# Kernel tuning notes

Measured on AMD Instinct MI355X. Metric: run time of the kernel, lower is better.

Reference implementation:

```python
import jax, jax.numpy as jnp
import numpy as np

B, S, E, H, F = 4, 2048, 1024, 16, 4096
D = E // H
EPS = 1e-5


def setup_inputs() -> dict:
    key = jax.random.key(0)
    ks = jax.random.split(key, 12)
    sc_e = 1.0 / np.sqrt(E)
    sc_f = 1.0 / np.sqrt(F)
    inp = {
        'x': jax.random.normal(ks[0], (B, S, E), jnp.float32),
        'mask': jnp.tril(jnp.ones((S, S), jnp.int32))[None, None],  # causal [1,1,S,S]
        'ln1_g': jnp.ones((E,), jnp.float32),
        'ln1_b': jnp.zeros((E,), jnp.float32),
        'Wq': jax.random.normal(ks[1], (E, E), jnp.float32) * sc_e,
        'bq': jnp.zeros((E,), jnp.float32),
        'Wk': jax.random.normal(ks[2], (E, E), jnp.float32) * sc_e,
        'bk': jnp.zeros((E,), jnp.float32),
        'Wv': jax.random.normal(ks[3], (E, E), jnp.float32) * sc_e,
        'bv': jnp.zeros((E,), jnp.float32),
        'Wo': jax.random.normal(ks[4], (E, E), jnp.float32) * sc_e,
        'bo': jnp.zeros((E,), jnp.float32),
        'ln2_g': jnp.ones((E,), jnp.float32),
        'ln2_b': jnp.zeros((E,), jnp.float32),
        'W1': jax.random.normal(ks[5], (F, E), jnp.float32) * sc_e,
        'b1': jnp.zeros((F,), jnp.float32),
        'W2': jax.random.normal(ks[6], (E, F), jnp.float32) * sc_f,
        'b2': jnp.zeros((E,), jnp.float32),
    }
    return inp


def _ln(x, g, b):
    m = jnp.mean(x, axis=-1, keepdims=True)
    v = jnp.mean(jnp.square(x - m), axis=-1, keepdims=True)
    return (x - m) * jax.lax.rsqrt(v + EPS) * g + b


def _attn(h, mask, Wq, bq, Wk, bk, Wv, bv, Wo, bo):
    b, s, _ = h.shape
    q = (h @ Wq.T + bq).reshape(b, s, H, D)
    k = (h @ Wk.T + bk).reshape(b, s, H, D)
    v = (h @ Wv.T + bv).reshape(b, s, H, D)
    scores = jnp.einsum('bqhd,bkhd->bhqk', q, k) / np.sqrt(D)
    scores = jnp.where(mask == 0, -jnp.inf, scores)
    w = jax.nn.softmax(scores, axis=-1)
    ctx = jnp.einsum('bhqk,bkhd->bqhd', w, v).reshape(b, s, E)
    return ctx @ Wo.T + bo


def reference(x, mask, ln1_g, ln1_b, Wq, bq, Wk, bk, Wv, bv, Wo, bo,
              ln2_g, ln2_b, W1, b1, W2, b2):
    x = x + _attn(_ln(x, ln1_g, ln1_b), mask, Wq, bq, Wk, bk, Wv, bv, Wo, bo)
    h = _ln(x, ln2_g, ln2_b)
    ffn = jax.nn.gelu(h @ W1.T + b1, approximate=False) @ W2.T + b2
    return x + ffn
```

## Files before the change

kernel.cpp:

```cpp
#include <hip/hip_runtime.h>
#include <cstdint>
#include <cstddef>

#define E_DIM 1024
#define F_DIM 4096
#define S_LEN 2048
#define NB    4
#define NH    16
#define HD    64
#define MROWS 8192

typedef __bf16 bf16x8 __attribute__((ext_vector_type(8)));
typedef float  f32x4  __attribute__((ext_vector_type(4)));

struct alignas(16) f4 { float x, y, z, w; };
__device__ __forceinline__ f4 ld4(const float* p){ return *(const f4*)p; }

__device__ __forceinline__ unsigned short f2bf(float f){
  union { float f; unsigned int u; } c; c.f = f;
  unsigned int u = c.u;
  return (unsigned short)((u + 0x7FFFu + ((u >> 16) & 1u)) >> 16);
}

__device__ __forceinline__ float gelu_fast(float v){
  const float x  = v * 0.70710678118654752f;
  const float ax = fabsf(x);
  const float t  = __builtin_amdgcn_rcpf(1.0f + 0.3275911f * ax);
  const float p  = t*(0.254829592f + t*(-0.284496736f + t*(1.421413741f +
                   t*(-1.453152027f + t*1.061405429f))));
  float er = 1.0f - p * __expf(-x * x);
  er = (x < 0.0f) ? -er : er;
  return 0.5f * v * (1.0f + er);
}

__device__ __forceinline__ void xcd_swz(int gx, int gy, int& bn, int& bm){
  int fid = blockIdx.y * gx + blockIdx.x;
  const int nwg = gx * gy;
  fid = (fid & 7) * (nwg >> 3) + (fid >> 3);
  bn = fid % gx; bm = fid / gx;
}

__global__ void cvt_kernel(const float* __restrict__ in, unsigned short* __restrict__ out,
                           int n, float scale){
  int i = (blockIdx.x * 256 + threadIdx.x) * 4;
  if (i >= n) return;
  f4 f = ld4(in + i);
  ushort4 o;
  o.x = f2bf(f.x * scale); o.y = f2bf(f.y * scale);
  o.z = f2bf(f.z * scale); o.w = f2bf(f.w * scale);
  *(ushort4*)(out + i) = o;
}

__global__ void bias_cat(const float* __restrict__ bq, const float* __restrict__ bk,
                         const float* __restrict__ bv, float* __restrict__ out, float qsc){
  int i = blockIdx.x * 256 + threadIdx.x;
  if (i >= 3 * E_DIM) return;
  float v = (i < E_DIM) ? bq[i] * qsc : (i < 2 * E_DIM ? bk[i - E_DIM] : bv[i - 2 * E_DIM]);
  out[i] = v;
}

__global__ __launch_bounds__(256) void ln_kernel(const float* __restrict__ in,
                                                 const float* __restrict__ g,
                                                 const float* __restrict__ b,
                                                 unsigned short* __restrict__ out){
  const int row = blockIdx.x;
  const int t = threadIdx.x;
  const float* xr = in + (size_t)row * E_DIM;
  f4 xv = ld4(xr + t * 4);
  float s  = xv.x + xv.y + xv.z + xv.w;
  float ss = xv.x*xv.x + xv.y*xv.y + xv.z*xv.z + xv.w*xv.w;
  #pragma unroll
  for (int o = 1; o < 64; o <<= 1){ s += __shfl_xor(s, o); ss += __shfl_xor(ss, o); }
  __shared__ float sa[4], sb[4];
  if ((t & 63) == 0){ sa[t >> 6] = s; sb[t >> 6] = ss; }
  __syncthreads();
  s  = sa[0] + sa[1] + sa[2] + sa[3];
  ss = sb[0] + sb[1] + sb[2] + sb[3];
  const float mean = s * (1.0f / E_DIM);
  const float var  = ss * (1.0f / E_DIM) - mean * mean;
  const float rstd = rsqrtf(var + 1e-5f);
  f4 gv = ld4(g + t * 4);
  f4 bv = ld4(b + t * 4);
  ushort4 o;
  o.x = f2bf((xv.x - mean) * rstd * gv.x + bv.x);
  o.y = f2bf((xv.y - mean) * rstd * gv.y + bv.y);
  o.z = f2bf((xv.z - mean) * rstd * gv.z + bv.z);
  o.w = f2bf((xv.w - mean) * rstd * gv.w + bv.w);
  *(ushort4*)(out + (size_t)row * E_DIM + t * 4) = o;
}

__device__ __forceinline__ void async_cp16(const unsigned short* g, unsigned short* l){
  __builtin_amdgcn_global_load_lds((const __attribute__((address_space(1))) unsigned int*)g,
                                   (__attribute__((address_space(3)))       unsigned int*)l,
                                   16, 0, 0);
}

template<int EPI>
__global__ __launch_bounds__(256) void gemm_bt(const unsigned short* __restrict__ A,
                                               const unsigned short* __restrict__ W,
                                               const float* __restrict__ bias,
                                               const float* __restrict__ res,
                                               void* __restrict__ outp,
                                               int M, int N, int K){
  __shared__ unsigned short As[128 * 64];
  __shared__ unsigned short Bs[128 * 64];
  int bn, bm; xcd_swz(gridDim.x, gridDim.y, bn, bm);
  const int tid = threadIdx.x;
  const int wv = tid >> 6, lane = tid & 63;
  const int lr = lane & 15, qd = lane >> 4;
  const int wm = (wv >> 1) * 64, wn = (wv & 1) * 64;

  f32x4 acc[4][4];
  #pragma unroll
  for (int mt = 0; mt < 4; ++mt)
    #pragma unroll
    for (int nt = 0; nt < 4; ++nt)
      acc[mt][nt] = f32x4{0.f, 0.f, 0.f, 0.f};

  int soff[4];
  int srow[4];
  #pragma unroll
  for (int it = 0; it < 4; ++it){
    const int cc = tid + it * 256;
    srow[it] = cc >> 3;
    soff[it] = (((cc & 7) ^ (srow[it] & 7))) * 8;
  }
  const unsigned short* Abase = A + (size_t)(bm * 128) * K;
  const unsigned short* Wbase = W + (size_t)(bn * 128) * K;

  for (int k0 = 0; k0 < K; k0 += 64){
    __syncthreads();
    #pragma unroll
    for (int it = 0; it < 4; ++it){
      async_cp16(Abase + (size_t)srow[it] * K + k0 + soff[it], &As[(tid + it * 256) * 8]);
      async_cp16(Wbase + (size_t)srow[it] * K + k0 + soff[it], &Bs[(tid + it * 256) * 8]);
    }
    __builtin_amdgcn_s_waitcnt(0);
    __syncthreads();

    #pragma unroll
    for (int kk = 0; kk < 2; ++kk){
      bf16x8 af[4], bf[4];
      #pragma unroll
      for (int mt = 0; mt < 4; ++mt){
        const int fr = wm + mt * 16 + lr;
        af[mt] = *(const bf16x8*)&As[fr * 64 + (((kk * 4 + qd) ^ (fr & 7))) * 8];
      }
      #pragma unroll
      for (int nt = 0; nt < 4; ++nt){
        const int fr = wn + nt * 16 + lr;
        bf[nt] = *(const bf16x8*)&Bs[fr * 64 + (((kk * 4 + qd) ^ (fr & 7))) * 8];
      }
      #pragma unroll
      for (int mt = 0; mt < 4; ++mt)
        #pragma unroll
        for (int nt = 0; nt < 4; ++nt)
          acc[mt][nt] = __builtin_amdgcn_mfma_f32_16x16x32_bf16(af[mt], bf[nt], acc[mt][nt], 0, 0, 0);
    }
  }

  #pragma unroll
  for (int mt = 0; mt < 4; ++mt){
    #pragma unroll
    for (int r = 0; r < 4; ++r){
      const int gm = bm * 128 + wm + mt * 16 + qd * 4 + r;
      const size_t rowoff = (size_t)gm * N;
      #pragma unroll
      for (int nt = 0; nt < 4; ++nt){
        const int gn = bn * 128 + wn + nt * 16 + lr;
        float v = acc[mt][nt][r] + bias[gn];
        if constexpr (EPI == 1) v = gelu_fast(v);
        if constexpr (EPI == 2) ((float*)outp)[rowoff + gn] = v + res[rowoff + gn];
        else                    ((unsigned short*)outp)[rowoff + gn] = f2bf(v);
      }
    }
  }
}

#define VMW4() asm volatile("s_waitcnt vmcnt(4)" ::: "memory")
#define VMW0() asm volatile("s_waitcnt vmcnt(0)" ::: "memory")
#define BAR()  __builtin_amdgcn_s_barrier()

template<int EPI>
__global__ __launch_bounds__(512, 2) void gemm256(const unsigned short* __restrict__ A,
                                                  const unsigned short* __restrict__ W,
                                                  const float* __restrict__ bias,
                                                  unsigned short* __restrict__ outp,
                                                  int M, int N, int K){
  __shared__ unsigned short lds[2][2][256 * 64];
  const int bn = blockIdx.x, bm = blockIdx.y;
  const int tid = threadIdx.x;
  const int lane = tid & 63;
  const int wv = tid >> 6;
  const int lr = lane & 15, qd = lane >> 4;
  const int wm = wv >> 2, wn = wv & 3;
  const int NT = K >> 6;

  f32x4 acc[2][2][4][2];
  #pragma unroll
  for (int a = 0; a < 2; ++a)
    #pragma unroll
    for (int b = 0; b < 2; ++b)
      #pragma unroll
      for (int c = 0; c < 4; ++c)
        #pragma unroll
        for (int d = 0; d < 2; ++d)
          acc[a][b][c][d] = f32x4{0.f, 0.f, 0.f, 0.f};

  const int srow = tid >> 3;
  const int scol = ((tid & 7) ^ (srow & 7)) * 8;
  const unsigned short* Ab = A + (size_t)(bm * 256 + srow) * K + scol;
  const unsigned short* Wb = W + (size_t)(bn * 256 + srow) * K + scol;

#define STAGE_A(bufi, h, kt) do{ \
    async_cp16(Ab + (size_t)((h)*128     ) * K + (size_t)(kt) * 64, &lds[bufi][0][((h)*128     ) * 64 + tid * 8]); \
    async_cp16(Ab + (size_t)((h)*128 + 64) * K + (size_t)(kt) * 64, &lds[bufi][0][((h)*128 + 64) * 64 + tid * 8]); \
  }while(0)
#define STAGE_B(bufi, h, kt) do{ \
    async_cp16(Wb + (size_t)((h)*128     ) * K + (size_t)(kt) * 64, &lds[bufi][1][((h)*128     ) * 64 + tid * 8]); \
    async_cp16(Wb + (size_t)((h)*128 + 64) * K + (size_t)(kt) * 64, &lds[bufi][1][((h)*128 + 64) * 64 + tid * 8]); \
  }while(0)

  const int sw0 = ((qd    ) ^ (lr & 7)) * 8;
  const int sw1 = ((qd + 4) ^ (lr & 7)) * 8;
  const int arow = wm * 64 + lr;
  const int brow = wn * 32 + lr;

  bf16x8 af[4][2], b0[2][2], b1[2][2];

#define LDA(bufi, mh) do{ \
    _Pragma("unroll") \
    for (int mt = 0; mt < 4; ++mt){ \
      const int r_ = (mh)*128 + arow + mt * 16; \
      af[mt][0] = *(const bf16x8*)&lds[bufi][0][r_ * 64 + sw0]; \
      af[mt][1] = *(const bf16x8*)&lds[bufi][0][r_ * 64 + sw1]; \
    } }while(0)
#define LDB(bufi, nh, dst) do{ \
    _Pragma("unroll") \
    for (int nt = 0; nt < 2; ++nt){ \
      const int r_ = (nh)*128 + brow + nt * 16; \
      dst[nt][0] = *(const bf16x8*)&lds[bufi][1][r_ * 64 + sw0]; \
      dst[nt][1] = *(const bf16x8*)&lds[bufi][1][r_ * 64 + sw1]; \
    } }while(0)
#define MMA(mh, nh, bfr) do{ \
    __builtin_amdgcn_s_setprio(1); \
    _Pragma("unroll") \
    for (int kk = 0; kk < 2; ++kk) \
      _Pragma("unroll") \
      for (int mt = 0; mt < 4; ++mt) \
        _Pragma("unroll") \
        for (int nt = 0; nt < 2; ++nt) \
          acc[mh][nh][mt][nt] = __builtin_amdgcn_mfma_f32_16x16x32_bf16(af[mt][kk], bfr[nt][kk], acc[mh][nh][mt][nt], 0, 0, 0); \
    __builtin_amdgcn_s_setprio(0); \
  }while(0)

  STAGE_A(0, 0, 0); STAGE_B(0, 1, 0); STAGE_A(0, 1, 0); STAGE_B(0, 0, 0);
  STAGE_A(1, 0, 1); STAGE_B(1, 1, 1);
  VMW4(); BAR();

  for (int t = 0; t < NT; t += 2){
    const bool s2 = (t + 2) < NT, s3 = (t + 3) < NT;
    LDA(0, 0); LDB(0, 0, b0);
    STAGE_A(1, 1, t + 1);
    BAR(); MMA(0, 0, b0);
    LDB(0, 1, b1);
    BAR();
    STAGE_B(1, 0, t + 1);
    BAR(); MMA(0, 1, b1);
    LDA(0, 1);
    BAR();
    if (s2) STAGE_A(0, 0, t + 2);
    BAR(); MMA(1, 1, b1); BAR();
    if (s2) STAGE_B(0, 1, t + 2);
    BAR(); MMA(1, 0, b0);
    if (s2) { VMW4(); } else { VMW0(); }
    LDA(1, 0);
    BAR();
    LDB(1, 0, b0);
    if (s2) STAGE_A(0, 1, t + 2);
    BAR(); MMA(0, 0, b0);
    LDB(1, 1, b1);
    BAR();
    if (s2) STAGE_B(0, 0, t + 2);
    BAR(); MMA(0, 1, b1);
    LDA(1, 1);
    BAR();
    if (s3) STAGE_A(1, 0, t + 3);
    BAR(); MMA(1, 1, b1); BAR();
    if (s3) STAGE_B(1, 1, t + 3);
    BAR(); MMA(1, 0, b0);
    VMW4();
    BAR();
  }

  #pragma unroll
  for (int mh = 0; mh < 2; ++mh)
    #pragma unroll
    for (int nh = 0; nh < 2; ++nh)
      #pragma unroll
      for (int mt = 0; mt < 4; ++mt){
        const int gm0 = bm * 256 + mh * 128 + wm * 64 + mt * 16 + qd * 4;
        #pragma unroll
        for (int r = 0; r < 4; ++r){
          const size_t rowoff = (size_t)(gm0 + r) * N;
          #pragma unroll
          for (int nt = 0; nt < 2; ++nt){
            const int gn = bn * 256 + nh * 128 + wn * 32 + nt * 16 + lr;
            float v = acc[mh][nh][mt][nt][r] + bias[gn];
            if constexpr (EPI == 1) v = gelu_fast(v);
            outp[rowoff + gn] = f2bf(v);
          }
        }
      }
#undef STAGE_A
#undef STAGE_B
#undef LDA
#undef LDB
#undef MMA
}

__global__ __launch_bounds__(256) void vtrans(const unsigned short* __restrict__ QKV,
                                              unsigned short* __restrict__ Vt){
  __shared__ unsigned short Ts[64 * 66];
  const int st = blockIdx.x;
  const int h = blockIdx.y, b = blockIdx.z;
  const int tid = threadIdx.x;
  const size_t srcbase = (size_t)(b * S_LEN + st * 64) * 3072 + 2 * E_DIM + h * HD;
  #pragma unroll
  for (int it = 0; it < 4; ++it){
    const int ch = tid + it * 256;
    const int row = ch >> 4, c4 = (ch & 15) * 4;
    *(ushort4*)&Ts[row * 66 + c4] = *(const ushort4*)(QKV + srcbase + (size_t)row * 3072 + c4);
  }
  __syncthreads();
  const size_t dstbase = (size_t)((b * NH + h) * HD) * S_LEN + st * 64;
  #pragma unroll
  for (int it = 0; it < 4; ++it){
    const int ch = tid + it * 256;
    const int d = ch >> 4, t4 = (ch & 15) * 4;
    ushort4 o;
    o.x = Ts[(t4 + 0) * 66 + d];
    o.y = Ts[(t4 + 1) * 66 + d];
    o.z = Ts[(t4 + 2) * 66 + d];
    o.w = Ts[(t4 + 3) * 66 + d];
    *(ushort4*)&Vt[dstbase + (size_t)d * S_LEN + t4] = o;
  }
}

#define AST 72
__global__ __launch_bounds__(256) void attn_mfma(const unsigned short* __restrict__ QKV,
                                                 const unsigned short* __restrict__ Vt,
                                                 unsigned short* __restrict__ Om){
  __shared__ unsigned short Ks[64 * 64];
  __shared__ unsigned short Vs[64 * 64];
  __shared__ unsigned short Ps[64 * AST];
  const int pairi = blockIdx.x;
  const int h = blockIdx.y, b = blockIdx.z;
  const int tid = threadIdx.x;
  const int w = tid >> 6, lane = tid & 63;
  const int lr = lane & 15, qd = lane >> 4;
  const size_t row0 = (size_t)b * S_LEN;
  const int qcol = h * HD;
  const int kcol = E_DIM + h * HD;
  const unsigned short* Vtb = Vt + (size_t)((b * NH + h) * HD) * S_LEN;

  const int sr  = tid >> 3;
  const int sc  = (((tid & 7) ^ (sr & 7))) * 8;
  const int sdst = sr * 64 + (tid & 7) * 8;

  bf16x8 ones;
  #pragma unroll
  for (int j = 0; j < 8; ++j) ones[j] = (__bf16)1.0f;

  for (int ph = 0; ph < 2; ++ph){
    const int qb_t = ph ? (31 - pairi) : pairi;
    const int q0 = qb_t * 64 + w * 16;

    bf16x8 qf[2];
    #pragma unroll
    for (int kk = 0; kk < 2; ++kk)
      qf[kk] = *(const bf16x8*)(QKV + (row0 + q0 + lr) * 3072 + qcol + kk * 32 + qd * 8);

    f32x4 accd[4];
    #pragma unroll
    for (int dt = 0; dt < 4; ++dt) accd[dt] = f32x4{0.f, 0.f, 0.f, 0.f};
    f32x4 lacc = f32x4{0.f, 0.f, 0.f, 0.f};

    uint4 k0r = *(const uint4*)(QKV + (row0 + sr) * 3072 + kcol + sc);
    uint4 k1r = *(const uint4*)(QKV + (row0 + sr + 32) * 3072 + kcol + sc);
    uint4 v0r = *(const uint4*)(Vtb + (size_t)sr * S_LEN + sc);
    uint4 v1r = *(const uint4*)(Vtb + (size_t)(sr + 32) * S_LEN + sc);

    for (int kt = 0; kt <= qb_t; ++kt){
      __syncthreads();
      *(uint4*)&Ks[sdst          ] = k0r;
      *(uint4*)&Ks[sdst + 32 * 64] = k1r;
      *(uint4*)&Vs[sdst          ] = v0r;
      *(uint4*)&Vs[sdst + 32 * 64] = v1r;
      if (kt < qb_t){
        const int kn = kt + 1;
        k0r = *(const uint4*)(QKV + (row0 + kn * 64 + sr) * 3072 + kcol + sc);
        k1r = *(const uint4*)(QKV + (row0 + kn * 64 + sr + 32) * 3072 + kcol + sc);
        v0r = *(const uint4*)(Vtb + (size_t)sr * S_LEN + kn * 64 + sc);
        v1r = *(const uint4*)(Vtb + (size_t)(sr + 32) * S_LEN + kn * 64 + sc);
      }
      __syncthreads();

      f32x4 s[4];
      #pragma unroll
      for (int nt = 0; nt < 4; ++nt) s[nt] = f32x4{0.f, 0.f, 0.f, 0.f};
      #pragma unroll
      for (int kk = 0; kk < 2; ++kk){
        bf16x8 kf[4];
        #pragma unroll
        for (int nt = 0; nt < 4; ++nt)
          kf[nt] = *(const bf16x8*)&Ks[(nt * 16 + lr) * 64 + (((kk * 4 + qd) ^ (lr & 7))) * 8];
        #pragma unroll
        for (int nt = 0; nt < 4; ++nt)
          s[nt] = __builtin_amdgcn_mfma_f32_16x16x32_bf16(qf[kk], kf[nt], s[nt], 0, 0, 0);
      }
      if (kt == qb_t){
        #pragma unroll
        for (int nt = 0; nt < 4; ++nt)
          #pragma unroll
          for (int r = 0; r < 4; ++r){
            const int q  = q0 + qd * 4 + r;
            const int ky = kt * 64 + nt * 16 + lr;
            if (ky > q) s[nt][r] = -3e38f;
          }
      }
      #pragma unroll
      for (int nt = 0; nt < 4; ++nt)
        #pragma unroll
        for (int r = 0; r < 4; ++r){
          union { float f; unsigned u; } cc;
          cc.f = exp2f(s[nt][r]);
          Ps[(w * 16 + qd * 4 + r) * AST + nt * 16 + lr] = (unsigned short)((cc.u + 0x8000u) >> 16);
        }
      __builtin_amdgcn_s_waitcnt(0xc07f);
      #pragma unroll
      for (int kk = 0; kk < 2; ++kk){
        bf16x8 pf = *(const bf16x8*)&Ps[(w * 16 + lr) * AST + kk * 32 + qd * 8];
        bf16x8 vf[4];
        #pragma unroll
        for (int dt = 0; dt < 4; ++dt)
          vf[dt] = *(const bf16x8*)&Vs[(dt * 16 + lr) * 64 + (((kk * 4 + qd) ^ (lr & 7))) * 8];
        #pragma unroll
        for (int dt = 0; dt < 4; ++dt)
          accd[dt] = __builtin_amdgcn_mfma_f32_16x16x32_bf16(pf, vf[dt], accd[dt], 0, 0, 0);
        lacc = __builtin_amdgcn_mfma_f32_16x16x32_bf16(pf, ones, lacc, 0, 0, 0);
      }
    }

    #pragma unroll
    for (int r = 0; r < 4; ++r){
      const float inv = 1.0f / lacc[r];
      const size_t ro = (row0 + q0 + qd * 4 + r) * E_DIM + qcol;
      #pragma unroll
      for (int dt = 0; dt < 4; ++dt)
        Om[ro + dt * 16 + lr] = f2bf(accd[dt][r] * inv);
    }
  }
}

extern "C" void kernel_launch(void* const* d_in, const int* in_sizes, int n_in,
                              void* d_out, int out_size, void* d_ws, size_t ws_size,
                              hipStream_t stream){
  const float* x    = (const float*)d_in[0];
  const float* ln1g = (const float*)d_in[2];
  const float* ln1b = (const float*)d_in[3];
  const float* Wq   = (const float*)d_in[4];
  const float* bq   = (const float*)d_in[5];
  const float* Wk   = (const float*)d_in[6];
  const float* bk   = (const float*)d_in[7];
  const float* Wv   = (const float*)d_in[8];
  const float* bv   = (const float*)d_in[9];
  const float* Wo   = (const float*)d_in[10];
  const float* bo   = (const float*)d_in[11];
  const float* ln2g = (const float*)d_in[12];
  const float* ln2b = (const float*)d_in[13];
  const float* W1   = (const float*)d_in[14];
  const float* b1   = (const float*)d_in[15];
  const float* W2   = (const float*)d_in[16];
  const float* b2   = (const float*)d_in[17];

  char* ws = (char*)d_ws;
  const size_t MB = 1024 * 1024;
  unsigned short* Wqkv_b = (unsigned short*)(ws + 0 * MB);
  unsigned short* Wo_b   = (unsigned short*)(ws + 6 * MB);
  unsigned short* W1_b   = (unsigned short*)(ws + 8 * MB);
  unsigned short* W2_b   = (unsigned short*)(ws + 16 * MB);
  unsigned short* qkvb   = (unsigned short*)(ws + 24 * MB);
  float*          bqkv   = (float*)(ws + 72 * MB);
  unsigned short* Vt_g   = (unsigned short*)(ws + 72 * MB);
  unsigned short* lnb    = (unsigned short*)(ws + 88 * MB);
  float*          xres   = (float*)(ws + 104 * MB);
  unsigned short* ffn1   = (unsigned short*)(ws + 24 * MB);
  unsigned short* ctxb   = lnb;

  const float QSC = 0.125f * 1.4426950408889634f;

  cvt_kernel<<<1024, 256, 0, stream>>>(Wq, Wqkv_b,                   E_DIM * E_DIM, QSC);
  cvt_kernel<<<1024, 256, 0, stream>>>(Wk, Wqkv_b + E_DIM * E_DIM,   E_DIM * E_DIM, 1.0f);
  cvt_kernel<<<1024, 256, 0, stream>>>(Wv, Wqkv_b + 2 * E_DIM * E_DIM, E_DIM * E_DIM, 1.0f);
  cvt_kernel<<<1024, 256, 0, stream>>>(Wo, Wo_b, E_DIM * E_DIM, 1.0f);
  cvt_kernel<<<4096, 256, 0, stream>>>(W1, W1_b, F_DIM * E_DIM, 1.0f);
  cvt_kernel<<<4096, 256, 0, stream>>>(W2, W2_b, F_DIM * E_DIM, 1.0f);
  bias_cat<<<12, 256, 0, stream>>>(bq, bk, bv, bqkv, QSC);

  ln_kernel<<<MROWS, 256, 0, stream>>>(x, ln1g, ln1b, lnb);

  gemm256<0><<<dim3(3 * E_DIM / 256, MROWS / 256), 512, 0, stream>>>(
      lnb, Wqkv_b, bqkv, qkvb, MROWS, 3 * E_DIM, E_DIM);

  vtrans<<<dim3(S_LEN / 64, NH, NB), 256, 0, stream>>>(qkvb, Vt_g);

  attn_mfma<<<dim3(16, NH, NB), 256, 0, stream>>>(qkvb, Vt_g, ctxb);

  gemm_bt<2><<<dim3(E_DIM / 128, MROWS / 128), 256, 0, stream>>>(
      ctxb, Wo_b, bo, x, xres, MROWS, E_DIM, E_DIM);

  ln_kernel<<<MROWS, 256, 0, stream>>>(xres, ln2g, ln2b, lnb);

  gemm256<1><<<dim3(F_DIM / 256, MROWS / 256), 512, 0, stream>>>(
      lnb, W1_b, b1, ffn1, MROWS, F_DIM, E_DIM);

  gemm_bt<2><<<dim3(E_DIM / 128, MROWS / 128), 256, 0, stream>>>(
      ffn1, W2_b, b2, xres, (float*)d_out, MROWS, E_DIM, F_DIM);
}
```

Baseline: 524.6 us.

## Replace residual GEMMs with double-buffered 256x128 pipelined MFMA kernel

Replaces the simple single-buffered 128x128 GEMM used for the output projection and FFN2 with a 256x128-tile, 512-thread kernel. It double-buffers LDS, interleaves async global-to-LDS loads with MFMA phases, and uses setprio around the MFMA blocks. The aim is to hide global load latency, which the old kernel exposed with a full waitcnt(0) every K step, and to get more reuse per tile. In exchange it halves the number of blocks (256 blocks with one block per CU by launch bounds), which may leave some CUs idle, and the barrier schedule is intricate.

```diff
diff --git a/kernel.cpp b/kernel.cpp
--- a/kernel.cpp
+++ b/kernel.cpp
@@ -95,88 +95,6 @@
                                    16, 0, 0);
 }
 
-template<int EPI>
-__global__ __launch_bounds__(256) void gemm_bt(const unsigned short* __restrict__ A,
-                                               const unsigned short* __restrict__ W,
-                                               const float* __restrict__ bias,
-                                               const float* __restrict__ res,
-                                               void* __restrict__ outp,
-                                               int M, int N, int K){
-  __shared__ unsigned short As[128 * 64];
-  __shared__ unsigned short Bs[128 * 64];
-  int bn, bm; xcd_swz(gridDim.x, gridDim.y, bn, bm);
-  const int tid = threadIdx.x;
-  const int wv = tid >> 6, lane = tid & 63;
-  const int lr = lane & 15, qd = lane >> 4;
-  const int wm = (wv >> 1) * 64, wn = (wv & 1) * 64;
-
-  f32x4 acc[4][4];
-  #pragma unroll
-  for (int mt = 0; mt < 4; ++mt)
-    #pragma unroll
-    for (int nt = 0; nt < 4; ++nt)
-      acc[mt][nt] = f32x4{0.f, 0.f, 0.f, 0.f};
-
-  int soff[4];
-  int srow[4];
-  #pragma unroll
-  for (int it = 0; it < 4; ++it){
-    const int cc = tid + it * 256;
-    srow[it] = cc >> 3;
-    soff[it] = (((cc & 7) ^ (srow[it] & 7))) * 8;
-  }
-  const unsigned short* Abase = A + (size_t)(bm * 128) * K;
-  const unsigned short* Wbase = W + (size_t)(bn * 128) * K;
-
-  for (int k0 = 0; k0 < K; k0 += 64){
-    __syncthreads();
-    #pragma unroll
-    for (int it = 0; it < 4; ++it){
-      async_cp16(Abase + (size_t)srow[it] * K + k0 + soff[it], &As[(tid + it * 256) * 8]);
-      async_cp16(Wbase + (size_t)srow[it] * K + k0 + soff[it], &Bs[(tid + it * 256) * 8]);
-    }
-    __builtin_amdgcn_s_waitcnt(0);
-    __syncthreads();
-
-    #pragma unroll
-    for (int kk = 0; kk < 2; ++kk){
-      bf16x8 af[4], bf[4];
-      #pragma unroll
-      for (int mt = 0; mt < 4; ++mt){
-        const int fr = wm + mt * 16 + lr;
-        af[mt] = *(const bf16x8*)&As[fr * 64 + (((kk * 4 + qd) ^ (fr & 7))) * 8];
-      }
-      #pragma unroll
-      for (int nt = 0; nt < 4; ++nt){
-        const int fr = wn + nt * 16 + lr;
-        bf[nt] = *(const bf16x8*)&Bs[fr * 64 + (((kk * 4 + qd) ^ (fr & 7))) * 8];
-      }
-      #pragma unroll
-      for (int mt = 0; mt < 4; ++mt)
-        #pragma unroll
-        for (int nt = 0; nt < 4; ++nt)
-          acc[mt][nt] = __builtin_amdgcn_mfma_f32_16x16x32_bf16(af[mt], bf[nt], acc[mt][nt], 0, 0, 0);
-    }
-  }
-
-  #pragma unroll
-  for (int mt = 0; mt < 4; ++mt){
-    #pragma unroll
-    for (int r = 0; r < 4; ++r){
-      const int gm = bm * 128 + wm + mt * 16 + qd * 4 + r;
-      const size_t rowoff = (size_t)gm * N;
-      #pragma unroll
-      for (int nt = 0; nt < 4; ++nt){
-        const int gn = bn * 128 + wn + nt * 16 + lr;
-        float v = acc[mt][nt][r] + bias[gn];
-        if constexpr (EPI == 1) v = gelu_fast(v);
-        if constexpr (EPI == 2) ((float*)outp)[rowoff + gn] = v + res[rowoff + gn];
-        else                    ((unsigned short*)outp)[rowoff + gn] = f2bf(v);
-      }
-    }
-  }
-}
-
 #define VMW4() asm volatile("s_waitcnt vmcnt(4)" ::: "memory")
 #define VMW0() asm volatile("s_waitcnt vmcnt(0)" ::: "memory")
 #define BAR()  __builtin_amdgcn_s_barrier()
@@ -317,6 +235,145 @@
 #undef LDA
 #undef LDB
 #undef MMA
+}
+
+__global__ __launch_bounds__(512, 1) void gemm256x128(const unsigned short* __restrict__ A,
+                                                      const unsigned short* __restrict__ W,
+                                                      const float* __restrict__ bias,
+                                                      const float* __restrict__ res,
+                                                      float* __restrict__ outp,
+                                                      int M, int N, int K){
+  __shared__ unsigned short As[2][256 * 64];
+  __shared__ unsigned short Bs[2][128 * 64];
+  int bn, bm; xcd_swz(gridDim.x, gridDim.y, bn, bm);
+  const int tid = threadIdx.x;
+  const int lane = tid & 63;
+  const int wv = tid >> 6;
+  const int lr = lane & 15, qd = lane >> 4;
+  const int wm = wv >> 1, wn = wv & 1;
+  const int NT = K >> 6;
+
+  f32x4 acc[4][4];
+  #pragma unroll
+  for (int a = 0; a < 4; ++a)
+    #pragma unroll
+    for (int b = 0; b < 4; ++b)
+      acc[a][b] = f32x4{0.f, 0.f, 0.f, 0.f};
+
+  const int srow = tid >> 3;
+  const int scol = ((tid & 7) ^ (srow & 7)) * 8;
+  const int sdst = srow * 64 + (tid & 7) * 8;
+  const unsigned short* Ab = A + (size_t)(bm * 256 + srow) * K + scol;
+  const unsigned short* Wb = W + (size_t)(bn * 128 + srow) * K + scol;
+
+#define XSTAGE_A(bufi, kt) do{ \
+    _Pragma("unroll") \
+    for (int h = 0; h < 4; ++h) \
+      async_cp16(Ab + (size_t)(h * 64) * K + (size_t)(kt) * 64, &As[bufi][h * 64 * 64 + sdst]); \
+  }while(0)
+#define XSTAGE_B(bufi, kt) do{ \
+    _Pragma("unroll") \
+    for (int h = 0; h < 2; ++h) \
+      async_cp16(Wb + (size_t)(h * 64) * K + (size_t)(kt) * 64, &Bs[bufi][h * 64 * 64 + sdst]); \
+  }while(0)
+
+  const int sw0 = ((qd    ) ^ (lr & 7)) * 8;
+  const int sw1 = ((qd + 4) ^ (lr & 7)) * 8;
+  const int arow = wm * 64 + lr;
+  const int brow = wn * 64 + lr;
+
+  bf16x8 af[4][2], b0[2][2], b1[2][2];
+
+#define XLDA(bufi) do{ \
+    _Pragma("unroll") \
+    for (int mt = 0; mt < 4; ++mt){ \
+      const int r_ = arow + mt * 16; \
+      af[mt][0] = *(const bf16x8*)&As[bufi][r_ * 64 + sw0]; \
+      af[mt][1] = *(const bf16x8*)&As[bufi][r_ * 64 + sw1]; \
+    } }while(0)
+#define XLDB0(bufi) do{ \
+    _Pragma("unroll") \
+    for (int j = 0; j < 2; ++j){ \
+      const int r_ = brow + j * 16; \
+      b0[j][0] = *(const bf16x8*)&Bs[bufi][r_ * 64 + sw0]; \
+      b0[j][1] = *(const bf16x8*)&Bs[bufi][r_ * 64 + sw1]; \
+    } }while(0)
+#define XLDB1(bufi) do{ \
+    _Pragma("unroll") \
+    for (int j = 0; j < 2; ++j){ \
+      const int r_ = brow + (2 + j) * 16; \
+      b1[j][0] = *(const bf16x8*)&Bs[bufi][r_ * 64 + sw0]; \
+      b1[j][1] = *(const bf16x8*)&Bs[bufi][r_ * 64 + sw1]; \
+    } }while(0)
+#define XMMA0() do{ \
+    __builtin_amdgcn_s_setprio(1); \
+    _Pragma("unroll") \
+    for (int kk = 0; kk < 2; ++kk) \
+      _Pragma("unroll") \
+      for (int mt = 0; mt < 4; ++mt) \
+        _Pragma("unroll") \
+        for (int j = 0; j < 2; ++j) \
+          acc[mt][j] = __builtin_amdgcn_mfma_f32_16x16x32_bf16(af[mt][kk], b0[j][kk], acc[mt][j], 0, 0, 0); \
+    __builtin_amdgcn_s_setprio(0); \
+  }while(0)
+#define XMMA1() do{ \
+    __builtin_amdgcn_s_setprio(1); \
+    _Pragma("unroll") \
+    for (int kk = 0; kk < 2; ++kk) \
+      _Pragma("unroll") \
+      for (int mt = 0; mt < 4; ++mt) \
+        _Pragma("unroll") \
+        for (int j = 0; j < 2; ++j) \
+          acc[mt][2 + j] = __builtin_amdgcn_mfma_f32_16x16x32_bf16(af[mt][kk], b1[j][kk], acc[mt][2 + j], 0, 0, 0); \
+    __builtin_amdgcn_s_setprio(0); \
+  }while(0)
+
+  XSTAGE_A(0, 0); XSTAGE_B(0, 0); XSTAGE_A(1, 1);
+  VMW4(); BAR();
+
+  for (int t = 0; t < NT; t += 2){
+    const bool s2 = (t + 2) < NT;
+    XLDA(0); XLDB0(0);
+    XSTAGE_B(1, t + 1);
+    BAR(); XMMA0();
+    XLDB1(0);
+    BAR();
+    if (s2) XSTAGE_A(0, t + 2);
+    BAR(); XMMA1();
+    if (s2) { VMW4(); } else { VMW0(); }
+    XLDA(1); XLDB0(1);
+    BAR();
+    if (s2) XSTAGE_B(0, t + 2);
+    BAR(); XMMA0();
+    XLDB1(1);
+    BAR();
+    if (s2) XSTAGE_A(1, t + 3);
+    BAR(); XMMA1();
+    if (s2) VMW4();
+    BAR();
+  }
+
+  #pragma unroll
+  for (int mt = 0; mt < 4; ++mt){
+    #pragma unroll
+    for (int r = 0; r < 4; ++r){
+      const int gm = bm * 256 + wm * 64 + mt * 16 + qd * 4 + r;
+      const size_t rowoff = (size_t)gm * N;
+      #pragma unroll
+      for (int nt = 0; nt < 4; ++nt){
+        const int gn = bn * 128 + wn * 64 + nt * 16 + lr;
+        const float v = acc[mt][nt][r] + bias[gn];
+        outp[rowoff + gn] = v + res[rowoff + gn];
+      }
+    }
+  }
+#undef XSTAGE_A
+#undef XSTAGE_B
+#undef XLDA
+#undef XLDB0
+#undef XLDB1
+#undef XMMA0
+#undef XMMA1
 }
 
 __global__ __launch_bounds__(256) void vtrans(const unsigned short* __restrict__ QKV,
@@ -517,7 +574,7 @@
 
   attn_mfma<<<dim3(16, NH, NB), 256, 0, stream>>>(qkvb, Vt_g, ctxb);
 
-  gemm_bt<2><<<dim3(E_DIM / 128, MROWS / 128), 256, 0, stream>>>(
+  gemm256x128<<<dim3(E_DIM / 128, MROWS / 256), 512, 0, stream>>>(
       ctxb, Wo_b, bo, x, xres, MROWS, E_DIM, E_DIM);
 
   ln_kernel<<<MROWS, 256, 0, stream>>>(xres, ln2g, ln2b, lnb);
@@ -525,6 +582,6 @@
   gemm256<1><<<dim3(F_DIM / 256, MROWS / 256), 512, 0, stream>>>(
       lnb, W1_b, b1, ffn1, MROWS, F_DIM, E_DIM);
 
-  gemm_bt<2><<<dim3(E_DIM / 128, MROWS / 128), 256, 0, stream>>>(
+  gemm256x128<<<dim3(E_DIM / 128, MROWS / 256), 512, 0, stream>>>(
       ffn1, W2_b, b2, xres, (float*)d_out, MROWS, E_DIM, F_DIM);
 }
```

Result: no change. 528.5 us (+0.7%).
